# Optimization experiments

Hardware: AMD Instinct MI355X
Metric: run time of the kernel (lower is better)

The kernel has to match this reference:

```python
import jax, jax.numpy as jnp
import numpy as np

G = 4            # groups
IN_G = 16        # input_dim // groups
OUT_G = 32       # output_dim // groups
DEG = 3          # legendre degree
K = 3            # kernel size
EPS = 1e-5       # InstanceNorm eps


def _conv(x, w):
    # NCHW x OIHW, stride 1, padding 1 (SAME-like for k=3)
    return jax.lax.conv_general_dilated(
        x, w, window_strides=(1, 1), padding=((1, 1), (1, 1)),
        dimension_numbers=('NCHW', 'OIHW', 'NCHW'))


def setup_inputs() -> dict:
    key = jax.random.key(0)
    kx, kb, kp = jax.random.split(key, 3)
    x = jax.random.normal(kx, (32, 64, 112, 112), dtype=jnp.float32)
    # base conv weights, one per group, kaiming-uniform-ish scale
    fan_b = IN_G * K * K
    base_w = jax.random.uniform(kb, (G, OUT_G, IN_G, K, K), dtype=jnp.float32,
                                minval=-1.0, maxval=1.0) * np.sqrt(3.0 / fan_b)
    fan_p = IN_G * (DEG + 1) * K * K
    poly_w = jax.random.uniform(kp, (G, OUT_G, IN_G * (DEG + 1), K, K), dtype=jnp.float32,
                                minval=-1.0, maxval=1.0) * np.sqrt(3.0 / fan_p)
    return {"x": x, "base_w": base_w, "poly_w": poly_w}


def _legendre_basis(xn, degree):
    # xn: [B, C, H, W] in [-1, 1]; returns [B, C*(degree+1), H, W]
    polys = [jnp.ones_like(xn), xn]
    for n in range(1, degree):
        pn = ((2.0 * n + 1.0) * xn * polys[-1] - n * polys[-2]) / (n + 1.0)
        polys.append(pn)
    return jnp.concatenate(polys, axis=1)


def _forward(x, base_w, poly_w):
    outs = []
    for g in range(G):  # small fixed loop over groups
        xg = x[:, g * IN_G:(g + 1) * IN_G]
        base = _conv(xg, base_w[g])
        mn, mx = jnp.min(xg), jnp.max(xg)
        xn = 2.0 * (xg - mn) / (mx - mn) - 1.0
        basis = _legendre_basis(xn, DEG)            # [B, IN_G*(DEG+1), H, W]
        y = base + _conv(basis, poly_w[g])          # [B, OUT_G, H, W]
        # InstanceNorm2d (affine=False): per-sample, per-channel over spatial
        mu = jnp.mean(y, axis=(2, 3), keepdims=True)
        var = jnp.var(y, axis=(2, 3), keepdims=True)
        yn = (y - mu) * jax.lax.rsqrt(var + EPS)
        outs.append(jax.nn.silu(yn))
    return jnp.concatenate(outs, axis=1)


def reference(x, base_w, poly_w):
    return _forward(x, base_w, poly_w)
```

## Files before the change

kernel.cpp:

```cpp
#include <hip/hip_runtime.h>
#include <hip/hip_bf16.h>

#define HW 112
#define HWHW 12544
#define NB 32
#define CIN 64
#define G 4
#define IN_G 16
#define OUT_G 32

typedef _Float16 f16;
typedef _Float16 f16x8 __attribute__((ext_vector_type(8)));
typedef _Float16 f16x4 __attribute__((ext_vector_type(4)));
typedef float f32x4 __attribute__((ext_vector_type(4)));

__device__ __forceinline__ unsigned enc_f32(float f) {
    unsigned u = __float_as_uint(f);
    return (u & 0x80000000u) ? ~u : (u | 0x80000000u);
}
__device__ __forceinline__ float dec_f32(unsigned k) {
    unsigned u = (k & 0x80000000u) ? (k & 0x7fffffffu) : ~k;
    return __uint_as_float(u);
}

__global__ void init_mm(unsigned* mm) {
    int i = threadIdx.x;
    if (i < 2 * G) mm[i] = (i & 1) ? 0u : 0xFFFFFFFFu;
}

__global__ __launch_bounds__(256) void minmax_kernel(const float* __restrict__ x,
                                                     unsigned* __restrict__ mm) {
    const int g = blockIdx.y;
    const int chunk = IN_G * HWHW;
    const int group_elems = NB * chunk;
    float lmin = 3.4e38f, lmax = -3.4e38f;
    int stride = gridDim.x * blockDim.x * 4;
    for (int i = (blockIdx.x * blockDim.x + threadIdx.x) * 4; i < group_elems; i += stride) {
        int n = i / chunk;
        int r = i - n * chunk;
        const float4 v = *(const float4*)(x + ((long long)n * CIN + g * IN_G) * HWHW + r);
        lmin = fminf(lmin, fminf(fminf(v.x, v.y), fminf(v.z, v.w)));
        lmax = fmaxf(lmax, fmaxf(fmaxf(v.x, v.y), fmaxf(v.z, v.w)));
    }
    for (int o = 32; o > 0; o >>= 1) {
        lmin = fminf(lmin, __shfl_down(lmin, o));
        lmax = fmaxf(lmax, __shfl_down(lmax, o));
    }
    __shared__ float smn[4], smx[4];
    int wid = threadIdx.x >> 6, lane = threadIdx.x & 63;
    if (lane == 0) { smn[wid] = lmin; smx[wid] = lmax; }
    __syncthreads();
    if (threadIdx.x == 0) {
        float m0 = fminf(fminf(smn[0], smn[1]), fminf(smn[2], smn[3]));
        float m1 = fmaxf(fmaxf(smx[0], smx[1]), fmaxf(smx[2], smx[3]));
        atomicMin(&mm[2 * g],     enc_f32(m0));
        atomicMax(&mm[2 * g + 1], enc_f32(m1));
    }
}

__global__ __launch_bounds__(256) void fold_kernel(const float* __restrict__ bw,
                                                   const float* __restrict__ pw,
                                                   const unsigned* __restrict__ mm,
                                                   f16* __restrict__ Wf) {
    int idx = blockIdx.x * 256 + threadIdx.x;
    if (idx >= G * OUT_G * IN_G * 9) return;
    int g  = idx / (OUT_G * IN_G * 9);
    int r  = idx - g * (OUT_G * IN_G * 9);
    int co = r / (IN_G * 9);
    int r2 = r - co * (IN_G * 9);
    int ci = r2 / 9, tap = r2 - (r2 / 9) * 9;

    const float mn = dec_f32(mm[2 * g]);
    const float mx = dec_f32(mm[2 * g + 1]);
    const float a = 2.0f / (mx - mn);
    const float b = -a * mn - 1.0f;

    const float bwv = bw[((g * OUT_G + co) * IN_G + ci) * 9 + tap];
    const float* pwb = pw + (size_t)(g * OUT_G + co) * 64 * 9;
    const float p0 = pwb[(0  + ci) * 9 + tap];
    const float p1 = pwb[(16 + ci) * 9 + tap];
    const float p2 = pwb[(32 + ci) * 9 + tap];
    const float p3 = pwb[(48 + ci) * 9 + tap];

    const float W0 = p0 + p1 * b + p2 * (1.5f * b * b - 0.5f) + p3 * (2.5f * b * b * b - 1.5f * b);
    const float W1 = bwv + p1 * a + p2 * (3.0f * a * b) + p3 * (7.5f * a * b * b - 1.5f * a);
    const float W2 = p2 * (1.5f * a * a) + p3 * (7.5f * a * a * b);
    const float W3 = p3 * (2.5f * a * a * a);

    f16x4 v; v[0] = (f16)W0; v[1] = (f16)W1; v[2] = (f16)W2; v[3] = (f16)W3;
    size_t off = ((size_t)((g * 9 + tap) * OUT_G + co)) * 64
               + (size_t)(((ci >> 1) ^ (co & 7)) * 8 + (ci & 1) * 4);
    *(f16x4*)(Wf + off) = v;
}

__global__ __launch_bounds__(256) void conv_mfma(const float* __restrict__ x,
                                                 const f16* __restrict__ Wf,
                                                 float* __restrict__ out) {
    const int tile = blockIdx.x, g = blockIdx.y, n = blockIdx.z;
    const int ty0 = (tile / 7) * 16, tx0 = (tile % 7) * 16;

    __shared__ __align__(16) char As[18 * 18 * 128];
    __shared__ __align__(16) char Ws[2][4096];

    const int tid = threadIdx.x;
    const float* xg = x + ((size_t)n * CIN + g * IN_G) * HWHW;
    const char* WfG = (const char*)(Wf + (size_t)g * 9 * 2048);

    *(uint4*)(&Ws[0][tid * 16]) = *(const uint4*)(WfG + tid * 16);

    for (int it = 0; it < 11; ++it) {
        int j = tid + it * 256;
        if (j < 2592) {
            int cip = j / 324, pxIdx = j - cip * 324;
            int py = pxIdx / 18, px = pxIdx - py * 18;
            int gy = ty0 + py - 1, gx = tx0 + px - 1;
            bool ok = (gy >= 0) & (gy < HW) & (gx >= 0) & (gx < HW);
            const float* src = xg + (size_t)(2 * cip) * HWHW + gy * HW + gx;
            float v0 = ok ? src[0] : 0.0f;
            float v1 = ok ? src[HWHW] : 0.0f;
            f16 one = ok ? (f16)1.0f : (f16)0.0f;
            f16x8 pk;
            pk[0] = one; pk[1] = (f16)v0; pk[2] = (f16)(v0 * v0); pk[3] = (f16)(v0 * v0 * v0);
            pk[4] = one; pk[5] = (f16)v1; pk[6] = (f16)(v1 * v1); pk[7] = (f16)(v1 * v1 * v1);
            *(f16x8*)(&As[pxIdx * 128 + ((cip ^ (px & 7)) << 4)]) = pk;
        }
    }
    __syncthreads();

    const int l = tid & 63, w = tid >> 6;
    const int lx = l & 15, qu = l >> 4;

    int aoff[3][2], boff[2][2];
#pragma unroll
    for (int kw = 0; kw < 3; ++kw)
#pragma unroll
        for (int k2 = 0; k2 < 2; ++k2) {
            int pxr = lx + kw;
            aoff[kw][k2] = pxr * 128 + (((qu + 4 * k2) ^ (pxr & 7)) << 4);
        }
#pragma unroll
    for (int cs = 0; cs < 2; ++cs)
#pragma unroll
        for (int k2 = 0; k2 < 2; ++k2)
            boff[cs][k2] = (lx + 16 * cs) * 128 + (((qu + 4 * k2) ^ (lx & 7)) << 4);

    f32x4 acc[4][2];
#pragma unroll
    for (int rr = 0; rr < 4; ++rr)
#pragma unroll
        for (int cs = 0; cs < 2; ++cs) acc[rr][cs] = (f32x4)0.0f;

#pragma unroll
    for (int tap = 0; tap < 9; ++tap) {
        uint4 wpre;
        if (tap < 8) wpre = *(const uint4*)(WfG + (tap + 1) * 4096 + tid * 16);
        const char* Wb = Ws[tap & 1];
        const int kh = tap / 3, kw = tap - kh * 3;

        f16x8 b00 = *(const f16x8*)(Wb + boff[0][0]);
        f16x8 b10 = *(const f16x8*)(Wb + boff[1][0]);
        f16x8 b01 = *(const f16x8*)(Wb + boff[0][1]);
        f16x8 b11 = *(const f16x8*)(Wb + boff[1][1]);
#pragma unroll
        for (int rr = 0; rr < 4; ++rr) {
            int row = (4 * w + rr + kh) * 2304;
            f16x8 a0 = *(const f16x8*)(As + row + aoff[kw][0]);
            f16x8 a1 = *(const f16x8*)(As + row + aoff[kw][1]);
            acc[rr][0] = __builtin_amdgcn_mfma_f32_16x16x32_f16(a0, b00, acc[rr][0], 0, 0, 0);
            acc[rr][1] = __builtin_amdgcn_mfma_f32_16x16x32_f16(a0, b10, acc[rr][1], 0, 0, 0);
            acc[rr][0] = __builtin_amdgcn_mfma_f32_16x16x32_f16(a1, b01, acc[rr][0], 0, 0, 0);
            acc[rr][1] = __builtin_amdgcn_mfma_f32_16x16x32_f16(a1, b11, acc[rr][1], 0, 0, 0);
        }
        if (tap < 8) *(uint4*)(&Ws[(tap + 1) & 1][tid * 16]) = wpre;
        __syncthreads();
    }

    const size_t ob = ((size_t)n * (G * OUT_G) + g * OUT_G) * HWHW;
#pragma unroll
    for (int rr = 0; rr < 4; ++rr) {
        const int y = ty0 + 4 * w + rr;
#pragma unroll
        for (int cs = 0; cs < 2; ++cs) {
            float* dst = out + ob + (size_t)(cs * 16 + lx) * HWHW + (size_t)y * HW + tx0 + qu * 4;
            *(f32x4*)dst = acc[rr][cs];
        }
    }
}

__global__ __launch_bounds__(256) void norm_kernel(float* __restrict__ out) {
    __shared__ float buf[HWHW];
    __shared__ float red[2][4];
    const long long nc = blockIdx.x;
    float* p = out + nc * HWHW;

    float s = 0.0f, ss = 0.0f;
    for (int i = threadIdx.x; i < HWHW / 4; i += 256) {
        float4 v = ((const float4*)p)[i];
        ((float4*)buf)[i] = v;
        s += v.x + v.y + v.z + v.w;
        ss += v.x * v.x + v.y * v.y + v.z * v.z + v.w * v.w;
    }
    for (int o = 32; o > 0; o >>= 1) {
        s  += __shfl_down(s, o);
        ss += __shfl_down(ss, o);
    }
    const int wid = threadIdx.x >> 6, lane = threadIdx.x & 63;
    if (lane == 0) { red[0][wid] = s; red[1][wid] = ss; }
    __syncthreads();
    if (threadIdx.x == 0) {
        float S  = red[0][0] + red[0][1] + red[0][2] + red[0][3];
        float SS = red[1][0] + red[1][1] + red[1][2] + red[1][3];
        float mu = S * (1.0f / HWHW);
        float var = SS * (1.0f / HWHW) - mu * mu;
        red[0][0] = mu;
        red[1][0] = rsqrtf(var + 1e-5f);
    }
    __syncthreads();
    const float mu = red[0][0], rs = red[1][0];
    for (int i = threadIdx.x; i < HWHW / 4; i += 256) {
        float4 v = ((float4*)buf)[i];
        v.x = (v.x - mu) * rs; v.x = v.x / (1.0f + __expf(-v.x));
        v.y = (v.y - mu) * rs; v.y = v.y / (1.0f + __expf(-v.y));
        v.z = (v.z - mu) * rs; v.z = v.z / (1.0f + __expf(-v.z));
        v.w = (v.w - mu) * rs; v.w = v.w / (1.0f + __expf(-v.w));
        ((float4*)p)[i] = v;
    }
}

extern "C" void kernel_launch(void* const* d_in, const int* in_sizes, int n_in,
                              void* d_out, int out_size, void* d_ws, size_t ws_size,
                              hipStream_t stream) {
    const float* x  = (const float*)d_in[0];
    const float* bw = (const float*)d_in[1];
    const float* pw = (const float*)d_in[2];
    float* out = (float*)d_out;
    unsigned* mm = (unsigned*)d_ws;
    f16* Wf = (f16*)((char*)d_ws + 1024);

    init_mm<<<1, 64, 0, stream>>>(mm);
    minmax_kernel<<<dim3(256, G), 256, 0, stream>>>(x, mm);
    fold_kernel<<<72, 256, 0, stream>>>(bw, pw, mm, Wf);
    conv_mfma<<<dim3(49, G, NB), 256, 0, stream>>>(x, Wf, out);
    norm_kernel<<<NB * G * OUT_G, 256, 0, stream>>>(out);
}
```

Baseline: 492.4 us.

## Fuse instance-norm statistics into conv epilogue and restructure conv into two channel halves

The conv kernel now accumulates per-channel sum and sum-of-squares in its epilogue, using shared and global atomics, so the separate norm pass only applies the normalization and SiLU. This drops one full read of the output. The conv stages input channels in two halves with a smaller LDS tile, keeps all 9 taps' weights in registers, and reuses each loaded A row across the kh taps. The minmax kernel now uses one block per plane. Risks include more register pressure from holding B[9][2], atomic contention, and the numerically weaker one-pass variance in fp32.

```diff
diff --git a/kernel.cpp b/kernel.cpp
--- a/kernel.cpp
+++ b/kernel.cpp
@@ -8,6 +8,7 @@
 #define G 4
 #define IN_G 16
 #define OUT_G 32
+#define NC (NB * G * OUT_G)
 
 typedef _Float16 f16;
 typedef _Float16 f16x8 __attribute__((ext_vector_type(8)));
@@ -23,22 +24,22 @@
     return __uint_as_float(u);
 }
 
-__global__ void init_mm(unsigned* mm) {
-    int i = threadIdx.x;
-    if (i < 2 * G) mm[i] = (i & 1) ? 0u : 0xFFFFFFFFu;
+__global__ __launch_bounds__(256) void init_kernel(unsigned* __restrict__ mm,
+                                                   float* __restrict__ stats) {
+    int i = blockIdx.x * 256 + threadIdx.x;
+    if (i < 2 * NC) stats[i] = 0.0f;
+    if (blockIdx.x == 0 && threadIdx.x < 2 * G)
+        mm[threadIdx.x] = (threadIdx.x & 1) ? 0u : 0xFFFFFFFFu;
 }
 
 __global__ __launch_bounds__(256) void minmax_kernel(const float* __restrict__ x,
                                                      unsigned* __restrict__ mm) {
-    const int g = blockIdx.y;
-    const int chunk = IN_G * HWHW;
-    const int group_elems = NB * chunk;
+    const int pc = blockIdx.x;
+    const int g = (pc & 63) >> 4;
+    const float* p = x + (size_t)pc * HWHW;
     float lmin = 3.4e38f, lmax = -3.4e38f;
-    int stride = gridDim.x * blockDim.x * 4;
-    for (int i = (blockIdx.x * blockDim.x + threadIdx.x) * 4; i < group_elems; i += stride) {
-        int n = i / chunk;
-        int r = i - n * chunk;
-        const float4 v = *(const float4*)(x + ((long long)n * CIN + g * IN_G) * HWHW + r);
+    for (int i = threadIdx.x; i < HWHW / 4; i += 256) {
+        float4 v = ((const float4*)p)[i];
         lmin = fminf(lmin, fminf(fminf(v.x, v.y), fminf(v.z, v.w)));
         lmax = fmaxf(lmax, fmaxf(fmaxf(v.x, v.y), fmaxf(v.z, v.w)));
     }
@@ -87,92 +88,107 @@
     const float W2 = p2 * (1.5f * a * a) + p3 * (7.5f * a * a * b);
     const float W3 = p3 * (2.5f * a * a * a);
 
+    const int h = ci >> 3, cil = ci & 7;
     f16x4 v; v[0] = (f16)W0; v[1] = (f16)W1; v[2] = (f16)W2; v[3] = (f16)W3;
-    size_t off = ((size_t)((g * 9 + tap) * OUT_G + co)) * 64
-               + (size_t)(((ci >> 1) ^ (co & 7)) * 8 + (ci & 1) * 4);
+    size_t off = ((size_t)(((g * 2 + h) * 9 + tap) * OUT_G + co)) * 32 + cil * 4;
     *(f16x4*)(Wf + off) = v;
+}
+
+__device__ __forceinline__ int swz(int p, int u) {
+    return p * 64 + ((u ^ (p & 3) ^ ((p >> 2) & 1)) << 4);
 }
 
 __global__ __launch_bounds__(256) void conv_mfma(const float* __restrict__ x,
                                                  const f16* __restrict__ Wf,
-                                                 float* __restrict__ out) {
+                                                 float* __restrict__ out,
+                                                 float* __restrict__ stats) {
     const int tile = blockIdx.x, g = blockIdx.y, n = blockIdx.z;
     const int ty0 = (tile / 7) * 16, tx0 = (tile % 7) * 16;
 
-    __shared__ __align__(16) char As[18 * 18 * 128];
-    __shared__ __align__(16) char Ws[2][4096];
+    __shared__ __align__(16) char As[324 * 64];
+    __shared__ float sred[2][32];
 
     const int tid = threadIdx.x;
-    const float* xg = x + ((size_t)n * CIN + g * IN_G) * HWHW;
-    const char* WfG = (const char*)(Wf + (size_t)g * 9 * 2048);
-
-    *(uint4*)(&Ws[0][tid * 16]) = *(const uint4*)(WfG + tid * 16);
-
-    for (int it = 0; it < 11; ++it) {
-        int j = tid + it * 256;
-        if (j < 2592) {
-            int cip = j / 324, pxIdx = j - cip * 324;
-            int py = pxIdx / 18, px = pxIdx - py * 18;
-            int gy = ty0 + py - 1, gx = tx0 + px - 1;
-            bool ok = (gy >= 0) & (gy < HW) & (gx >= 0) & (gx < HW);
-            const float* src = xg + (size_t)(2 * cip) * HWHW + gy * HW + gx;
-            float v0 = ok ? src[0] : 0.0f;
-            float v1 = ok ? src[HWHW] : 0.0f;
-            f16 one = ok ? (f16)1.0f : (f16)0.0f;
-            f16x8 pk;
-            pk[0] = one; pk[1] = (f16)v0; pk[2] = (f16)(v0 * v0); pk[3] = (f16)(v0 * v0 * v0);
-            pk[4] = one; pk[5] = (f16)v1; pk[6] = (f16)(v1 * v1); pk[7] = (f16)(v1 * v1 * v1);
-            *(f16x8*)(&As[pxIdx * 128 + ((cip ^ (px & 7)) << 4)]) = pk;
-        }
-    }
-    __syncthreads();
-
     const int l = tid & 63, w = tid >> 6;
     const int lx = l & 15, qu = l >> 4;
 
-    int aoff[3][2], boff[2][2];
-#pragma unroll
-    for (int kw = 0; kw < 3; ++kw)
-#pragma unroll
-        for (int k2 = 0; k2 < 2; ++k2) {
-            int pxr = lx + kw;
-            aoff[kw][k2] = pxr * 128 + (((qu + 4 * k2) ^ (pxr & 7)) << 4);
-        }
-#pragma unroll
-    for (int cs = 0; cs < 2; ++cs)
-#pragma unroll
-        for (int k2 = 0; k2 < 2; ++k2)
-            boff[cs][k2] = (lx + 16 * cs) * 128 + (((qu + 4 * k2) ^ (lx & 7)) << 4);
+    if (tid < 64) ((float*)sred)[tid] = 0.0f;
+
+    const float* xg = x + ((size_t)n * CIN + g * IN_G) * HWHW;
+    const f16* WfG = Wf + (size_t)g * 2 * 9 * 1024;
 
     f32x4 acc[4][2];
 #pragma unroll
     for (int rr = 0; rr < 4; ++rr)
 #pragma unroll
-        for (int cs = 0; cs < 2; ++cs) acc[rr][cs] = (f32x4)0.0f;
-
-#pragma unroll
-    for (int tap = 0; tap < 9; ++tap) {
-        uint4 wpre;
-        if (tap < 8) wpre = *(const uint4*)(WfG + (tap + 1) * 4096 + tid * 16);
-        const char* Wb = Ws[tap & 1];
-        const int kh = tap / 3, kw = tap - kh * 3;
-
-        f16x8 b00 = *(const f16x8*)(Wb + boff[0][0]);
-        f16x8 b10 = *(const f16x8*)(Wb + boff[1][0]);
-        f16x8 b01 = *(const f16x8*)(Wb + boff[0][1]);
-        f16x8 b11 = *(const f16x8*)(Wb + boff[1][1]);
-#pragma unroll
-        for (int rr = 0; rr < 4; ++rr) {
-            int row = (4 * w + rr + kh) * 2304;
-            f16x8 a0 = *(const f16x8*)(As + row + aoff[kw][0]);
-            f16x8 a1 = *(const f16x8*)(As + row + aoff[kw][1]);
-            acc[rr][0] = __builtin_amdgcn_mfma_f32_16x16x32_f16(a0, b00, acc[rr][0], 0, 0, 0);
-            acc[rr][1] = __builtin_amdgcn_mfma_f32_16x16x32_f16(a0, b10, acc[rr][1], 0, 0, 0);
-            acc[rr][0] = __builtin_amdgcn_mfma_f32_16x16x32_f16(a1, b01, acc[rr][0], 0, 0, 0);
-            acc[rr][1] = __builtin_amdgcn_mfma_f32_16x16x32_f16(a1, b11, acc[rr][1], 0, 0, 0);
-        }
-        if (tap < 8) *(uint4*)(&Ws[(tap + 1) & 1][tid * 16]) = wpre;
+        for (int c = 0; c < 2; ++c) acc[rr][c] = (f32x4)0.0f;
+
+#pragma unroll
+    for (int h = 0; h < 2; ++h) {
+        f16x8 B[9][2];
+#pragma unroll
+        for (int t = 0; t < 9; ++t)
+#pragma unroll
+            for (int c = 0; c < 2; ++c)
+                B[t][c] = *(const f16x8*)(WfG + ((size_t)((h * 9 + t) * 32 + c * 16 + lx)) * 32 + qu * 8);
+
+        for (int it = 0; it < 6; ++it) {
+            int j = tid + it * 256;
+            if (j < 1296) {
+                int cip = j / 324, p = j - cip * 324;
+                int py = p / 18, px_ = p - py * 18;
+                int gy = ty0 + py - 1, gx = tx0 + px_ - 1;
+                bool ok = (gy >= 0) & (gy < HW) & (gx >= 0) & (gx < HW);
+                const float* src = xg + (size_t)(h * 8 + 2 * cip) * HWHW + gy * HW + gx;
+                float v0 = ok ? src[0] : 0.0f;
+                float v1 = ok ? src[HWHW] : 0.0f;
+                f16 one = ok ? (f16)1.0f : (f16)0.0f;
+                f16x8 pk;
+                pk[0] = one; pk[1] = (f16)v0; pk[2] = (f16)(v0 * v0); pk[3] = (f16)(v0 * v0 * v0);
+                pk[4] = one; pk[5] = (f16)v1; pk[6] = (f16)(v1 * v1); pk[7] = (f16)(v1 * v1 * v1);
+                *(f16x8*)(&As[swz(p, cip)]) = pk;
+            }
+        }
         __syncthreads();
+
+#pragma unroll
+        for (int kw = 0; kw < 3; ++kw) {
+            f16x8 a[6];
+#pragma unroll
+            for (int r = 0; r < 6; ++r) {
+                int pl = (4 * w + r) * 18 + lx + kw;
+                a[r] = *(const f16x8*)(&As[swz(pl, qu)]);
+            }
+#pragma unroll
+            for (int r = 0; r < 6; ++r)
+#pragma unroll
+                for (int kh = 0; kh < 3; ++kh) {
+                    const int rr = r - kh;
+                    if (rr >= 0 && rr < 4) {
+                        acc[rr][0] = __builtin_amdgcn_mfma_f32_16x16x32_f16(a[r], B[kh * 3 + kw][0], acc[rr][0], 0, 0, 0);
+                        acc[rr][1] = __builtin_amdgcn_mfma_f32_16x16x32_f16(a[r], B[kh * 3 + kw][1], acc[rr][1], 0, 0, 0);
+                    }
+                }
+        }
+        __syncthreads();
+    }
+
+    float s0 = 0.f, ss0 = 0.f, s1 = 0.f, ss1 = 0.f;
+#pragma unroll
+    for (int rr = 0; rr < 4; ++rr)
+#pragma unroll
+        for (int j = 0; j < 4; ++j) {
+            float v0 = acc[rr][0][j], v1 = acc[rr][1][j];
+            s0 += v0; ss0 += v0 * v0;
+            s1 += v1; ss1 += v1 * v1;
+        }
+    s0 += __shfl_xor(s0, 16); ss0 += __shfl_xor(ss0, 16);
+    s0 += __shfl_xor(s0, 32); ss0 += __shfl_xor(ss0, 32);
+    s1 += __shfl_xor(s1, 16); ss1 += __shfl_xor(ss1, 16);
+    s1 += __shfl_xor(s1, 32); ss1 += __shfl_xor(ss1, 32);
+    if (qu == 0) {
+        atomicAdd(&sred[0][lx],      s0); atomicAdd(&sred[1][lx],      ss0);
+        atomicAdd(&sred[0][16 + lx], s1); atomicAdd(&sred[1][16 + lx], ss1);
     }
 
     const size_t ob = ((size_t)n * (G * OUT_G) + g * OUT_G) * HWHW;
@@ -180,45 +196,30 @@
     for (int rr = 0; rr < 4; ++rr) {
         const int y = ty0 + 4 * w + rr;
 #pragma unroll
-        for (int cs = 0; cs < 2; ++cs) {
-            float* dst = out + ob + (size_t)(cs * 16 + lx) * HWHW + (size_t)y * HW + tx0 + qu * 4;
-            *(f32x4*)dst = acc[rr][cs];
-        }
-    }
-}
-
-__global__ __launch_bounds__(256) void norm_kernel(float* __restrict__ out) {
-    __shared__ float buf[HWHW];
-    __shared__ float red[2][4];
-    const long long nc = blockIdx.x;
-    float* p = out + nc * HWHW;
-
-    float s = 0.0f, ss = 0.0f;
+        for (int c = 0; c < 2; ++c) {
+            float* dst = out + ob + (size_t)(c * 16 + lx) * HWHW + (size_t)y * HW + tx0 + qu * 4;
+            *(f32x4*)dst = acc[rr][c];
+        }
+    }
+
+    __syncthreads();
+    if (tid < 32) {
+        const size_t slot = (size_t)n * (G * OUT_G) + g * OUT_G + tid;
+        atomicAdd(&stats[slot * 2],     sred[0][tid]);
+        atomicAdd(&stats[slot * 2 + 1], sred[1][tid]);
+    }
+}
+
+__global__ __launch_bounds__(256) void apply_kernel(float* __restrict__ out,
+                                                    const float* __restrict__ stats) {
+    const int nc = blockIdx.x;
+    const float s  = stats[nc * 2];
+    const float ss = stats[nc * 2 + 1];
+    const float mu = s * (1.0f / HWHW);
+    const float rs = rsqrtf(ss * (1.0f / HWHW) - mu * mu + 1e-5f);
+    float* p = out + (size_t)nc * HWHW;
     for (int i = threadIdx.x; i < HWHW / 4; i += 256) {
         float4 v = ((const float4*)p)[i];
-        ((float4*)buf)[i] = v;
-        s += v.x + v.y + v.z + v.w;
-        ss += v.x * v.x + v.y * v.y + v.z * v.z + v.w * v.w;
-    }
-    for (int o = 32; o > 0; o >>= 1) {
-        s  += __shfl_down(s, o);
-        ss += __shfl_down(ss, o);
-    }
-    const int wid = threadIdx.x >> 6, lane = threadIdx.x & 63;
-    if (lane == 0) { red[0][wid] = s; red[1][wid] = ss; }
-    __syncthreads();
-    if (threadIdx.x == 0) {
-        float S  = red[0][0] + red[0][1] + red[0][2] + red[0][3];
-        float SS = red[1][0] + red[1][1] + red[1][2] + red[1][3];
-        float mu = S * (1.0f / HWHW);
-        float var = SS * (1.0f / HWHW) - mu * mu;
-        red[0][0] = mu;
-        red[1][0] = rsqrtf(var + 1e-5f);
-    }
-    __syncthreads();
-    const float mu = red[0][0], rs = red[1][0];
-    for (int i = threadIdx.x; i < HWHW / 4; i += 256) {
-        float4 v = ((float4*)buf)[i];
         v.x = (v.x - mu) * rs; v.x = v.x / (1.0f + __expf(-v.x));
         v.y = (v.y - mu) * rs; v.y = v.y / (1.0f + __expf(-v.y));
         v.z = (v.z - mu) * rs; v.z = v.z / (1.0f + __expf(-v.z));
@@ -234,12 +235,14 @@
     const float* bw = (const float*)d_in[1];
     const float* pw = (const float*)d_in[2];
     float* out = (float*)d_out;
+
     unsigned* mm = (unsigned*)d_ws;
-    f16* Wf = (f16*)((char*)d_ws + 1024);
-
-    init_mm<<<1, 64, 0, stream>>>(mm);
-    minmax_kernel<<<dim3(256, G), 256, 0, stream>>>(x, mm);
-    fold_kernel<<<72, 256, 0, stream>>>(bw, pw, mm, Wf);
-    conv_mfma<<<dim3(49, G, NB), 256, 0, stream>>>(x, Wf, out);
-    norm_kernel<<<NB * G * OUT_G, 256, 0, stream>>>(out);
-}
+    float* stats = (float*)((char*)d_ws + 1024);
+    f16* Wf = (f16*)((char*)d_ws + 34816);
+
+    init_kernel<<<32, 256, 0, stream>>>(mm, stats);
+    minmax_kernel<<<NB * CIN, 256, 0, stream>>>(x, mm);
+    fold_kernel<<<144, 256, 0, stream>>>(bw, pw, mm, Wf);
+    conv_mfma<<<dim3(49, G, NB), 256, 0, stream>>>(x, Wf, out, stats);
+    apply_kernel<<<NC, 256, 0, stream>>>(out, stats);
+}
```

Result: slower. 522.4 us (+6.1%).
